# Kernel tuning notes

Measured on AMD Instinct MI355X. Metric: run time of the kernel, lower is better.

Reference implementation:

```python
import jax, jax.numpy as jnp
import numpy as np
from jax import lax

# Production-scale RPN detection-head config
B, FH, FW, NA = 8, 200, 200, 9      # batch, fmap h, fmap w, anchors/cell
H, W = 800, 800                      # image dims
N = FH * FW * NA                     # 360k anchors per image
NMS_THR = 0.7
MIN_SIZE = 1e-3


def _make_anchors():
    scales = np.array([32.0, 64.0, 128.0])
    ratios = np.array([0.5, 1.0, 2.0])
    ws = (scales[:, None] * np.sqrt(1.0 / ratios)[None, :]).reshape(-1)  # [NA]
    hs = (scales[:, None] * np.sqrt(ratios)[None, :]).reshape(-1)
    sy, sx = H / FH, W / FW
    cx = (np.arange(FW) + 0.5) * sx
    cy = (np.arange(FH) + 0.5) * sy
    cxg, cyg = np.meshgrid(cx, cy)                     # [FH,FW]
    cxg = cxg[..., None]; cyg = cyg[..., None]         # [FH,FW,1]
    a = np.stack([cxg - ws / 2, cyg - hs / 2, cxg + ws / 2, cyg + hs / 2], axis=-1)
    return jnp.asarray(a.reshape(-1, 4), jnp.float32)  # [N,4] xyxy


def setup_inputs() -> dict:
    key = jax.random.key(0)
    k1, k2 = jax.random.split(key)
    cls_logits = jax.random.normal(k1, (B, N, 1), jnp.float32)
    reg_deltas = jax.random.normal(k2, (B, N, 4), jnp.float32) * 0.1  # sane exp(dw)
    anchors = jnp.broadcast_to(_make_anchors()[None], (B, N, 4))
    return {
        "cls_logits": cls_logits,
        "reg_deltas": reg_deltas,
        "anchors": anchors,
        "keep_pre_nms": 1000,
        "keep_post_nms": 300,
    }


def _offsets2boxes(deltas, anchors):
    aw = anchors[:, 2] - anchors[:, 0]
    ah = anchors[:, 3] - anchors[:, 1]
    acx = anchors[:, 0] + 0.5 * aw
    acy = anchors[:, 1] + 0.5 * ah
    cx = deltas[:, 0] * aw + acx
    cy = deltas[:, 1] * ah + acy
    w = jnp.exp(deltas[:, 2]) * aw
    h = jnp.exp(deltas[:, 3]) * ah
    return jnp.stack([cx - 0.5 * w, cy - 0.5 * h, cx + 0.5 * w, cy + 0.5 * h], axis=-1)


def _iou_matrix(b):
    area = (b[:, 2] - b[:, 0]) * (b[:, 3] - b[:, 1])
    lt = jnp.maximum(b[:, None, :2], b[None, :, :2])
    rb = jnp.minimum(b[:, None, 2:], b[None, :, 2:])
    wh = jnp.clip(rb - lt, 0.0)
    inter = wh[..., 0] * wh[..., 1]
    return inter / (area[:, None] + area[None, :] - inter + 1e-9)


def _detect_one(logit, delta, anc, pre, post):
    scores = jax.nn.sigmoid(logit.reshape(-1))             # [N]
    boxes = _offsets2boxes(delta.reshape(-1, 4), anc)      # [N,4]
    s, idx = lax.top_k(scores, pre)                        # sorted desc
    b = boxes[idx]                                         # [pre,4]
    # clip to image
    b = jnp.stack([
        jnp.clip(b[:, 0], 0.0, W), jnp.clip(b[:, 1], 0.0, H),
        jnp.clip(b[:, 2], 0.0, W), jnp.clip(b[:, 3], 0.0, H)], axis=-1)
    valid = ((b[:, 2] - b[:, 0]) >= MIN_SIZE) & ((b[:, 3] - b[:, 1]) >= MIN_SIZE)
    # greedy NMS on score-sorted boxes (mask-based, fixed shapes)
    iou = _iou_matrix(lax.stop_gradient(b))                # [pre,pre]
    j = jnp.arange(pre)

    def body(keep, i):
        sup = (iou[i] > NMS_THR) & (j > i) & keep[i]
        return keep & ~sup, None

    keep, _ = lax.scan(body, valid, jnp.arange(pre))
    # compact first `post` kept detections into fixed [post,5], zero-padded
    dets = jnp.concatenate([b, s[:, None]], axis=-1)       # [pre,5]
    rank = jnp.cumsum(keep) - 1
    tgt = jnp.where(keep & (rank < post), rank, post)
    out = jnp.zeros((post + 1, 5), dets.dtype).at[tgt].set(dets)[:post]
    return out


def reference(cls_logits, reg_deltas, anchors, keep_pre_nms, keep_post_nms):
    f = lambda l, d, a: _detect_one(l, d, a, keep_pre_nms, keep_post_nms)
    return jax.vmap(f)(cls_logits, reg_deltas, anchors)    # [B,post,5]
```

## Files before the change

kernel.cpp:

```cpp
#include <hip/hip_runtime.h>
#include <stdint.h>
#include <math.h>

typedef unsigned long long u64;
typedef unsigned int u32;

#define NPI   360000
#define B_IMG 8
#define PRE   1000
#define POST  300
#define CAP   4096
#define NMSF  0.7f
#define IMG_W 800.0f
#define IMG_H 800.0f

#define NBIN    4096
#define KSHIFT  20
#define NGRP    64
#define CHUNK_H 30
#define F4PB_H  (NPI / 4 / CHUNK_H)
#define CHUNK_C 48
#define F4PB_C  (NPI / 4 / CHUNK_C)
#define EPB_C   (NPI / CHUNK_C)
#define LBUF    1024

#define CNT_OFF     0
#define VALID_OFF   256
#define PHIST_OFF   4096
#define PCOARSE_OFF 3936256
#define BOX_OFF     3997696
#define SCORE_OFF   4125696
#define CAND_OFF    4157696
#define MASK_OFF    4419840

#define LDSROWS 496
#define NMS_T   320
#define RBLK    16

__device__ __forceinline__ u32 fkey(float f) {
  u32 u = __float_as_uint(f);
  return (u & 0x80000000u) ? ~u : (u | 0x80000000u);
}
__device__ __forceinline__ u64 rl64(u64 v, int lane) {
  u32 lo = (u32)__builtin_amdgcn_readlane((int)(u32)v, lane);
  u32 hi = (u32)__builtin_amdgcn_readlane((int)(u32)(v >> 32), lane);
  return ((u64)hi << 32) | lo;
}
__device__ __forceinline__ u64 sx64(u64 v, int m) {
  u32 lo = (u32)__shfl_xor((int)(u32)v, m, 64);
  u32 hi = (u32)__shfl_xor((int)(u32)(v >> 32), m, 64);
  return ((u64)hi << 32) | lo;
}

__global__ __launch_bounds__(256) void k_hist(const float* __restrict__ logits,
                                              u32* __restrict__ phist,
                                              u32* __restrict__ pcoarse,
                                              u32* __restrict__ cnt,
                                              u64* __restrict__ validw) {
  __shared__ u32 h[4 * NBIN];
  const int img = blockIdx.y, c = blockIdx.x;
  const int tid = threadIdx.x;
  for (int i = tid; i < 4 * NBIN; i += 256) h[i] = 0;
  __syncthreads();
  const int salt = ((tid >> 4) & 3) * NBIN;
  const float4* L = (const float4*)(logits + (size_t)img * NPI) + (size_t)c * F4PB_H;
  for (int i = tid; i < F4PB_H; i += 256) {
    float4 v = L[i];
    atomicAdd(&h[salt + (fkey(v.x) >> KSHIFT)], 1u);
    atomicAdd(&h[salt + (fkey(v.y) >> KSHIFT)], 1u);
    atomicAdd(&h[salt + (fkey(v.z) >> KSHIFT)], 1u);
    atomicAdd(&h[salt + (fkey(v.w) >> KSHIFT)], 1u);
  }
  __syncthreads();
  u32* P = phist + ((size_t)img * CHUNK_H + c) * NBIN;
  u32* PC = pcoarse + ((size_t)img * CHUNK_H + c) * NGRP;
  const int lane = tid & 63;
#pragma unroll
  for (int k = 0; k < NBIN / 256; k++) {
    int i = k * 256 + tid;
    u32 v = h[i] + h[NBIN + i] + h[2 * NBIN + i] + h[3 * NBIN + i];
    P[i] = v;
    u32 s = v;
#pragma unroll
    for (int m = 1; m < 64; m <<= 1) s += (u32)__shfl_xor((int)s, m, 64);
    if (lane == 0) PC[i >> 6] = s;
  }
  if (c == 0) {
    if (tid < 16) validw[img * 16 + tid] = 0;
    if (img == 0 && tid < B_IMG) cnt[tid] = 0;
  }
}

__global__ __launch_bounds__(256) void k_compact(const float* __restrict__ logits,
                                                 const u32* __restrict__ phist,
                                                 const u32* __restrict__ pcoarse,
                                                 u32* __restrict__ cnt,
                                                 u64* __restrict__ cand) {
  __shared__ u64 buf[LBUF];
  __shared__ u32 bcnt;
  __shared__ u32 gbase;
  __shared__ int stb;
  const int img = blockIdx.y, c = blockIdx.x;
  const int t = threadIdx.x;
  if (t == 0) { bcnt = 0; stb = 0; }
  const float4* L = (const float4*)(logits + (size_t)img * NPI) + (size_t)c * F4PB_C;
  float4 r[8];
#pragma unroll
  for (int k = 0; k < 8; k++) {
    int i = t + k * 256;
    if (i < F4PB_C) r[k] = L[i];
  }
  if (t < 64) {
    const u32* PC = pcoarse + (size_t)img * CHUNK_H * NGRP;
    u32 cg = 0;
    for (int cc = 0; cc < CHUNK_H; cc++) cg += PC[cc * NGRP + t];
    u32 suf = cg;
#pragma unroll
    for (int off = 1; off < 64; off <<= 1) {
      u32 o = (u32)__shfl_down((int)suf, off, 64);
      if (t + off < 64) suf += o;
    }
    u32 sx = suf - cg;
    u64 bal = __ballot(suf >= (u32)PRE && sx < (u32)PRE);
    if (bal) {
      int gc = __builtin_ctzll(bal);
      u32 s_above = (u32)__shfl((int)sx, gc, 64);
      const u32* P = phist + (size_t)img * CHUNK_H * NBIN + gc * (NBIN / NGRP);
      u32 fb = 0;
      for (int cc = 0; cc < CHUNK_H; cc++) fb += P[(size_t)cc * NBIN + t];
      u32 fsuf = fb;
#pragma unroll
      for (int off = 1; off < 64; off <<= 1) {
        u32 o = (u32)__shfl_down((int)fsuf, off, 64);
        if (t + off < 64) fsuf += o;
      }
      u32 fincl = fsuf + s_above;
      u32 fexcl = fincl - fb;
      if (fincl >= (u32)PRE && fexcl < (u32)PRE) stb = gc * (NBIN / NGRP) + t;
    }
  }
  __syncthreads();
  const int tb = stb;
  const int ebase = c * EPB_C;
#pragma unroll
  for (int k = 0; k < 8; k++) {
    int i = t + k * 256;
    if (i < F4PB_C) {
      float xs[4] = {r[k].x, r[k].y, r[k].z, r[k].w};
#pragma unroll
      for (int q = 0; q < 4; q++) {
        float x = xs[q];
        if ((int)(fkey(x) >> KSHIFT) >= tb) {
          float ef = (float)exp(-(double)x);
          float sg = 1.0f / (1.0f + ef);
          u32 e = (u32)(ebase + 4 * i + q);
          u32 p = atomicAdd(&bcnt, 1u);
          if (p < LBUF)
            buf[p] = ((u64)fkey(sg) << 32) | (u64)(0xFFFFFFFFu - e);
        }
      }
    }
  }
  __syncthreads();
  if (t == 0) {
    u32 m = bcnt < LBUF ? bcnt : LBUF;
    bcnt = m;
    gbase = atomicAdd(&cnt[img], m);
  }
  __syncthreads();
  const u32 m = bcnt, gb = gbase;
  for (u32 j = t; j < m; j += 256) {
    u32 pos = gb + j;
    if (pos < CAP) cand[img * CAP + pos] = buf[j];
  }
}

__device__ __forceinline__ void emit_row(
    int img, int row, u64 key,
    const float* __restrict__ deltas, const float* __restrict__ anchors,
    float4* __restrict__ boxes, float* __restrict__ scores, u64* __restrict__ validw) {
  u32 hi  = (u32)(key >> 32);
  u32 idx = 0xFFFFFFFFu - (u32)(key & 0xFFFFFFFFu);
  u32 su  = (hi & 0x80000000u) ? (hi ^ 0x80000000u) : ~hi;
  float sc = __uint_as_float(su);
  size_t off = (size_t)img * NPI + idx;
  float4 d = ((const float4*)deltas)[off];
  float4 a = ((const float4*)anchors)[off];
  float aw = a.z - a.x, ah = a.w - a.y;
  float acx = a.x + 0.5f * aw, acy = a.y + 0.5f * ah;
  float cx = d.x * aw + acx, cy = d.y * ah + acy;
  float w = expf(d.z) * aw, h = expf(d.w) * ah;
  float x1 = cx - 0.5f * w, y1 = cy - 0.5f * h;
  float x2 = cx + 0.5f * w, y2 = cy + 0.5f * h;
  x1 = fminf(fmaxf(x1, 0.f), IMG_W);
  y1 = fminf(fmaxf(y1, 0.f), IMG_H);
  x2 = fminf(fmaxf(x2, 0.f), IMG_W);
  y2 = fminf(fmaxf(y2, 0.f), IMG_H);
  boxes[img * PRE + row]  = make_float4(x1, y1, x2, y2);
  scores[img * PRE + row] = sc;
  if (((x2 - x1) >= 1e-3f) && ((y2 - y1) >= 1e-3f))
    atomicOr(&validw[img * 16 + (row >> 6)], 1ull << (row & 63));
}

__global__ __launch_bounds__(256) void k_rank(
    const float* __restrict__ deltas, const float* __restrict__ anchors,
    const u32* __restrict__ cnt, const u64* __restrict__ cand,
    float4* __restrict__ boxes, float* __restrict__ scores, u64* __restrict__ validw) {
  __shared__ u64 skey[CAP];
  __shared__ u32 pc[4][256];
  const int img = blockIdx.y;
  int n = (int)cnt[img];
  if (n > CAP) n = CAP;
  const int base = blockIdx.x * 256;
  if (base >= n) return;
  for (int i = threadIdx.x; i < n; i += 256) skey[i] = cand[img * CAP + i];
  __syncthreads();
  const int w = threadIdx.x >> 6, l = threadIdx.x & 63;
  const int r0 = base + l, r1 = r0 + 64, r2 = r0 + 128, r3 = r0 + 192;
  u64 k0 = (r0 < n) ? skey[r0] : 0ull;
  u64 k1 = (r1 < n) ? skey[r1] : 0ull;
  u64 k2 = (r2 < n) ? skey[r2] : 0ull;
  u64 k3 = (r3 < n) ? skey[r3] : 0ull;
  int c0 = 0, c1 = 0, c2 = 0, c3 = 0;
  const int js = (w * n) >> 2, je = ((w + 1) * n) >> 2;
  for (int j = js; j < je; j++) {
    u64 kj = skey[j];
    c0 += (kj > k0); c1 += (kj > k1); c2 += (kj > k2); c3 += (kj > k3);
  }
  pc[w][l]       = (u32)c0;
  pc[w][l + 64]  = (u32)c1;
  pc[w][l + 128] = (u32)c2;
  pc[w][l + 192] = (u32)c3;
  __syncthreads();
  const int t = threadIdx.x;
  const int rr = base + t;
  if (rr < n) {
    int c = (int)(pc[0][t] + pc[1][t] + pc[2][t] + pc[3][t]);
    if (c < PRE) emit_row(img, c, skey[rr], deltas, anchors, boxes, scores, validw);
  }
}

__global__ __launch_bounds__(1024) void k_iou(const float4* __restrict__ boxes,
                                              u64* __restrict__ mask) {
  __shared__ float4 sb[1024];
  __shared__ float  sa[1024];
  const int img = blockIdx.y;
  const int tid = threadIdx.x;
  {
    float4 b = (tid < PRE) ? boxes[img * PRE + tid]
                           : make_float4(0.f, 0.f, 0.f, 0.f);
    sb[tid] = b;
    sa[tid] = (b.z - b.x) * (b.w - b.y);
  }
  __syncthreads();
  const int lane = tid & 63;
  const int wv   = tid >> 6;
  const int i    = blockIdx.x * 64 + lane;
  const bool rowok = (i < PRE);
  const float4 bi = sb[blockIdx.x * 64 + lane];
  const float  ai = sa[blockIdx.x * 64 + lane];
  const int cbase = wv << 6;
  u64 bits = 0;
#pragma unroll
  for (int k = 0; k < 64; k++) {
    int c = cbase + k;
    float4 bc = sb[c];
    float ac  = sa[c];
    float ltx = fmaxf(bi.x, bc.x), lty = fmaxf(bi.y, bc.y);
    float rbx = fminf(bi.z, bc.z), rby = fminf(bi.w, bc.w);
    float iw = fmaxf(rbx - ltx, 0.f), ih = fmaxf(rby - lty, 0.f);
    float inter = iw * ih;
    float iou = inter / (ai + ac - inter + 1e-9f);
    bits |= (iou > NMSF) ? (1ull << k) : 0ull;
  }
  int d = i - cbase;
  u64 gtmask = (d < 0) ? ~0ull : ((d >= 63) ? 0ull : (~0ull << (d + 1)));
  int rem = PRE - cbase;
  u64 tmask = (rem >= 64) ? ~0ull : ((rem <= 0) ? 0ull : ((1ull << rem) - 1ull));
  bits &= gtmask & tmask;
  if (rowok) mask[((size_t)img * PRE + i) * 16 + wv] = bits;
}

__global__ __launch_bounds__(NMS_T) void k_nms(
    const u64* __restrict__ mask, const u64* __restrict__ validw,
    const float4* __restrict__ boxes, const float* __restrict__ scores,
    float* __restrict__ out) {
  __shared__ u64 smask[LDSROWS * 16];
  __shared__ int skeeplist[POST];
  __shared__ int skept;
  const int img = blockIdx.x;
  const int tid = threadIdx.x;
  const u64* M = mask + (size_t)img * PRE * 16;
  u64 diag[16];
  if (tid < 64) {
#pragma unroll
    for (int cc = 0; cc < 16; cc++) {
      int row = cc * 64 + tid;
      diag[cc] = (row < PRE) ? M[(size_t)row * 16 + cc] : 0ull;
    }
  }
  for (int e = tid; e < LDSROWS * 16; e += NMS_T) smask[e] = M[e];
  __syncthreads();
  if (tid < 64) {
    const int lane = tid;
    const int w = lane & 15, g = lane >> 4;
    u64 rem = ~0ull;
    if (lane < 16) {
      rem = ~validw[img * 16 + lane];
      if (lane == 15) rem |= 0xFFFFFF0000000000ull;
    }
    int kept = 0;
#pragma unroll
    for (int cc = 0; cc < 16; cc++) {
      u64 alive = ~rl64(rem, cc);
      int kept0 = kept;
      while (alive != 0ull && kept < POST) {
        int r = __builtin_ctzll(alive);
        if (lane == 0) skeeplist[kept] = cc * 64 + r;
        kept++;
        u64 sup = rl64(diag[cc], r);
        alive &= ~sup;
        alive &= ~(1ull << r);
      }
      int nc = kept - kept0;
      if (nc > 0 && kept < POST && cc < 15) {
        u64 part = 0;
        for (int j = g; j < nc; j += 4) {
          int row = skeeplist[kept0 + j];
          part |= (row < LDSROWS) ? smask[row * 16 + w] : M[(size_t)row * 16 + w];
        }
        part |= sx64(part, 16);
        part |= sx64(part, 32);
        rem |= part;
      }
      if (kept >= POST) break;
    }
    if (lane == 0) skept = kept;
  }
  __syncthreads();
  if (tid < POST) {
    float4 bx = make_float4(0.f, 0.f, 0.f, 0.f);
    float  sc = 0.f;
    if (tid < skept) {
      int i = skeeplist[tid];
      bx = boxes[img * PRE + i];
      sc = scores[img * PRE + i];
    }
    float* o = out + ((size_t)img * POST + tid) * 5;
    o[0] = bx.x; o[1] = bx.y; o[2] = bx.z; o[3] = bx.w; o[4] = sc;
  }
}

extern "C" void kernel_launch(void* const* d_in, const int* in_sizes, int n_in,
                              void* d_out, int out_size, void* d_ws, size_t ws_size,
                              hipStream_t stream) {
  const float* logits  = (const float*)d_in[0];
  const float* deltas  = (const float*)d_in[1];
  const float* anchors = (const float*)d_in[2];
  float* out = (float*)d_out;
  char* ws = (char*)d_ws;

  u32* cnt      = (u32*)(ws + CNT_OFF);
  u64* validw   = (u64*)(ws + VALID_OFF);
  u32* phist    = (u32*)(ws + PHIST_OFF);
  u32* pcoarse  = (u32*)(ws + PCOARSE_OFF);
  float4* boxes = (float4*)(ws + BOX_OFF);
  float* scores = (float*)(ws + SCORE_OFF);
  u64* cand     = (u64*)(ws + CAND_OFF);
  u64* mask     = (u64*)(ws + MASK_OFF);

  dim3 gh(CHUNK_H, B_IMG);
  k_hist<<<gh, 256, 0, stream>>>(logits, phist, pcoarse, cnt, validw);
  dim3 gc(CHUNK_C, B_IMG);
  k_compact<<<gc, 256, 0, stream>>>(logits, phist, pcoarse, cnt, cand);
  dim3 gr(RBLK, B_IMG);
  k_rank<<<gr, 256, 0, stream>>>(deltas, anchors, cnt, cand, boxes, scores, validw);
  dim3 g2(16, B_IMG);
  k_iou<<<g2, 1024, 0, stream>>>(boxes, mask);
  k_nms<<<B_IMG, NMS_T, 0, stream>>>(mask, validw, boxes, scores, out);
}
```

Before: 210.2 us.

## Replace histogram threshold pass with fixed logit threshold and exact fallback

Removes the per-image histogram kernel. Candidates are now selected with a fixed logit threshold and written into per-block buffers. The rank kernel gathers these buffers, and if any block overflows or the total falls outside the range needed for the top 1000, it rebuilds the exact histogram and threshold in-kernel. The IoU kernel is re-gridded to 32-row blocks and zeroes mask words strictly below the diagonal without computing them. This cuts a full pass over the logits and a launch, at the cost of a slow single-block fallback if the input distribution differs.

New measurement: 200.4 us. -4.7%, faster.

```diff
diff --git a/kernel.cpp b/kernel.cpp
--- a/kernel.cpp
+++ b/kernel.cpp
@@ -17,21 +17,19 @@
 #define NBIN    4096
 #define KSHIFT  20
 #define NGRP    64
-#define CHUNK_H 30
-#define F4PB_H  (NPI / 4 / CHUNK_H)
 #define CHUNK_C 48
 #define F4PB_C  (NPI / 4 / CHUNK_C)
 #define EPB_C   (NPI / CHUNK_C)
-#define LBUF    1024
-
-#define CNT_OFF     0
+#define PBLK    128
+
+#define THR_LOGIT 2.62f
+
 #define VALID_OFF   256
-#define PHIST_OFF   4096
-#define PCOARSE_OFF 3936256
-#define BOX_OFF     3997696
-#define SCORE_OFF   4125696
-#define CAND_OFF    4157696
-#define MASK_OFF    4419840
+#define BCNT_OFF    4096
+#define PCAND_OFF   8192
+#define BOX_OFF     401408
+#define SCORE_OFF   529408
+#define MASK_OFF    561408
 
 #define LDSROWS 496
 #define NMS_T   320
@@ -52,127 +50,42 @@
   return ((u64)hi << 32) | lo;
 }
 
-__global__ __launch_bounds__(256) void k_hist(const float* __restrict__ logits,
-                                              u32* __restrict__ phist,
-                                              u32* __restrict__ pcoarse,
-                                              u32* __restrict__ cnt,
-                                              u64* __restrict__ validw) {
-  __shared__ u32 h[4 * NBIN];
-  const int img = blockIdx.y, c = blockIdx.x;
-  const int tid = threadIdx.x;
-  for (int i = tid; i < 4 * NBIN; i += 256) h[i] = 0;
-  __syncthreads();
-  const int salt = ((tid >> 4) & 3) * NBIN;
-  const float4* L = (const float4*)(logits + (size_t)img * NPI) + (size_t)c * F4PB_H;
-  for (int i = tid; i < F4PB_H; i += 256) {
-    float4 v = L[i];
-    atomicAdd(&h[salt + (fkey(v.x) >> KSHIFT)], 1u);
-    atomicAdd(&h[salt + (fkey(v.y) >> KSHIFT)], 1u);
-    atomicAdd(&h[salt + (fkey(v.z) >> KSHIFT)], 1u);
-    atomicAdd(&h[salt + (fkey(v.w) >> KSHIFT)], 1u);
-  }
-  __syncthreads();
-  u32* P = phist + ((size_t)img * CHUNK_H + c) * NBIN;
-  u32* PC = pcoarse + ((size_t)img * CHUNK_H + c) * NGRP;
-  const int lane = tid & 63;
-#pragma unroll
-  for (int k = 0; k < NBIN / 256; k++) {
-    int i = k * 256 + tid;
-    u32 v = h[i] + h[NBIN + i] + h[2 * NBIN + i] + h[3 * NBIN + i];
-    P[i] = v;
-    u32 s = v;
-#pragma unroll
-    for (int m = 1; m < 64; m <<= 1) s += (u32)__shfl_xor((int)s, m, 64);
-    if (lane == 0) PC[i >> 6] = s;
-  }
-  if (c == 0) {
-    if (tid < 16) validw[img * 16 + tid] = 0;
-    if (img == 0 && tid < B_IMG) cnt[tid] = 0;
-  }
-}
-
 __global__ __launch_bounds__(256) void k_compact(const float* __restrict__ logits,
-                                                 const u32* __restrict__ phist,
-                                                 const u32* __restrict__ pcoarse,
-                                                 u32* __restrict__ cnt,
-                                                 u64* __restrict__ cand) {
-  __shared__ u64 buf[LBUF];
+                                                 u32* __restrict__ bcnt_blk,
+                                                 u64* __restrict__ pcand,
+                                                 u64* __restrict__ validw) {
   __shared__ u32 bcnt;
-  __shared__ u32 gbase;
-  __shared__ int stb;
   const int img = blockIdx.y, c = blockIdx.x;
   const int t = threadIdx.x;
-  if (t == 0) { bcnt = 0; stb = 0; }
+  const u32 FK0 = fkey(THR_LOGIT);
+  if (t == 0) bcnt = 0;
+  if (c == 0 && t < 16) validw[img * 16 + t] = 0;
+  __syncthreads();
   const float4* L = (const float4*)(logits + (size_t)img * NPI) + (size_t)c * F4PB_C;
-  float4 r[8];
-#pragma unroll
-  for (int k = 0; k < 8; k++) {
-    int i = t + k * 256;
-    if (i < F4PB_C) r[k] = L[i];
-  }
-  if (t < 64) {
-    const u32* PC = pcoarse + (size_t)img * CHUNK_H * NGRP;
-    u32 cg = 0;
-    for (int cc = 0; cc < CHUNK_H; cc++) cg += PC[cc * NGRP + t];
-    u32 suf = cg;
-#pragma unroll
-    for (int off = 1; off < 64; off <<= 1) {
-      u32 o = (u32)__shfl_down((int)suf, off, 64);
-      if (t + off < 64) suf += o;
-    }
-    u32 sx = suf - cg;
-    u64 bal = __ballot(suf >= (u32)PRE && sx < (u32)PRE);
-    if (bal) {
-      int gc = __builtin_ctzll(bal);
-      u32 s_above = (u32)__shfl((int)sx, gc, 64);
-      const u32* P = phist + (size_t)img * CHUNK_H * NBIN + gc * (NBIN / NGRP);
-      u32 fb = 0;
-      for (int cc = 0; cc < CHUNK_H; cc++) fb += P[(size_t)cc * NBIN + t];
-      u32 fsuf = fb;
-#pragma unroll
-      for (int off = 1; off < 64; off <<= 1) {
-        u32 o = (u32)__shfl_down((int)fsuf, off, 64);
-        if (t + off < 64) fsuf += o;
-      }
-      u32 fincl = fsuf + s_above;
-      u32 fexcl = fincl - fb;
-      if (fincl >= (u32)PRE && fexcl < (u32)PRE) stb = gc * (NBIN / NGRP) + t;
-    }
-  }
-  __syncthreads();
-  const int tb = stb;
+  u64* P = pcand + ((size_t)img * CHUNK_C + c) * PBLK;
   const int ebase = c * EPB_C;
 #pragma unroll
   for (int k = 0; k < 8; k++) {
     int i = t + k * 256;
     if (i < F4PB_C) {
-      float xs[4] = {r[k].x, r[k].y, r[k].z, r[k].w};
+      float4 v = L[i];
+      float xs[4] = {v.x, v.y, v.z, v.w};
 #pragma unroll
       for (int q = 0; q < 4; q++) {
         float x = xs[q];
-        if ((int)(fkey(x) >> KSHIFT) >= tb) {
+        if (fkey(x) >= FK0) {
           float ef = (float)exp(-(double)x);
           float sg = 1.0f / (1.0f + ef);
           u32 e = (u32)(ebase + 4 * i + q);
           u32 p = atomicAdd(&bcnt, 1u);
-          if (p < LBUF)
-            buf[p] = ((u64)fkey(sg) << 32) | (u64)(0xFFFFFFFFu - e);
+          if (p < PBLK)
+            P[p] = ((u64)fkey(sg) << 32) | (u64)(0xFFFFFFFFu - e);
         }
       }
     }
   }
   __syncthreads();
-  if (t == 0) {
-    u32 m = bcnt < LBUF ? bcnt : LBUF;
-    bcnt = m;
-    gbase = atomicAdd(&cnt[img], m);
-  }
-  __syncthreads();
-  const u32 m = bcnt, gb = gbase;
-  for (u32 j = t; j < m; j += 256) {
-    u32 pos = gb + j;
-    if (pos < CAP) cand[img * CAP + pos] = buf[j];
-  }
+  if (t == 0) bcnt_blk[img * CHUNK_C + c] = bcnt;
 }
 
 __device__ __forceinline__ void emit_row(
@@ -203,19 +116,114 @@
 }
 
 __global__ __launch_bounds__(256) void k_rank(
+    const float* __restrict__ logits,
     const float* __restrict__ deltas, const float* __restrict__ anchors,
-    const u32* __restrict__ cnt, const u64* __restrict__ cand,
+    const u32* __restrict__ bcnt_blk, const u64* __restrict__ pcand,
     float4* __restrict__ boxes, float* __restrict__ scores, u64* __restrict__ validw) {
   __shared__ u64 skey[CAP];
   __shared__ u32 pc[4][256];
+  __shared__ u32 scnt[CHUNK_C], soff[CHUNK_C];
+  __shared__ int sn, sbad, stb;
+  __shared__ u32 rc;
   const int img = blockIdx.y;
-  int n = (int)cnt[img];
-  if (n > CAP) n = CAP;
+  const int tid = threadIdx.x;
+  const int w = tid >> 6, l = tid & 63;
+  if (tid < CHUNK_C) scnt[tid] = bcnt_blk[img * CHUNK_C + tid];
+  if (tid == 0) { sbad = 0; stb = 0; rc = 0; }
+  __syncthreads();
+  if (tid < 64) {
+    u32 m = (tid < CHUNK_C) ? (scnt[tid] > (u32)PBLK ? (u32)PBLK : scnt[tid]) : 0u;
+    u64 bb = __ballot(tid < CHUNK_C && scnt[tid] > (u32)PBLK);
+    u32 x = m;
+#pragma unroll
+    for (int off = 1; off < 64; off <<= 1) {
+      u32 o = (u32)__shfl_up((int)x, off, 64);
+      if (l >= off) x += o;
+    }
+    if (tid < CHUNK_C) soff[tid] = x - m;
+    u32 tot = (u32)__builtin_amdgcn_readlane((int)x, 63);
+    if (tid == 0) {
+      sn = (int)tot;
+      if (bb != 0ull || tot < (u32)PRE || tot > (u32)CAP) sbad = 1;
+    }
+  }
+  __syncthreads();
+  int n = sn;
+  if (!sbad) {
+    for (int c = w; c < CHUNK_C; c += 4) {
+      u32 mc = scnt[c];
+      u32 off = soff[c];
+      const u64* src = pcand + ((size_t)img * CHUNK_C + c) * PBLK;
+      for (u32 j = l; j < mc; j += 64) skey[off + j] = src[j];
+    }
+    __syncthreads();
+  } else {
+    u32* hh = (u32*)skey;
+    for (int i = tid; i < NBIN; i += 256) hh[i] = 0;
+    __syncthreads();
+    const float4* L = (const float4*)(logits + (size_t)img * NPI);
+    for (int i = tid; i < NPI / 4; i += 256) {
+      float4 v = L[i];
+      atomicAdd(&hh[fkey(v.x) >> KSHIFT], 1u);
+      atomicAdd(&hh[fkey(v.y) >> KSHIFT], 1u);
+      atomicAdd(&hh[fkey(v.z) >> KSHIFT], 1u);
+      atomicAdd(&hh[fkey(v.w) >> KSHIFT], 1u);
+    }
+    __syncthreads();
+    if (tid < 64) {
+      u32 cg = 0;
+      for (int b = 0; b < NBIN / NGRP; b++) cg += hh[tid * (NBIN / NGRP) + b];
+      u32 suf = cg;
+#pragma unroll
+      for (int off = 1; off < 64; off <<= 1) {
+        u32 o = (u32)__shfl_down((int)suf, off, 64);
+        if (tid + off < 64) suf += o;
+      }
+      u32 sx = suf - cg;
+      u64 bal = __ballot(suf >= (u32)PRE && sx < (u32)PRE);
+      if (bal) {
+        int gc = __builtin_ctzll(bal);
+        u32 s_above = (u32)__shfl((int)sx, gc, 64);
+        u32 fb = hh[gc * (NBIN / NGRP) + tid];
+        u32 fsuf = fb;
+#pragma unroll
+        for (int off = 1; off < 64; off <<= 1) {
+          u32 o = (u32)__shfl_down((int)fsuf, off, 64);
+          if (tid + off < 64) fsuf += o;
+        }
+        u32 fincl = fsuf + s_above, fexcl = fincl - fb;
+        if (fincl >= (u32)PRE && fexcl < (u32)PRE) stb = gc * (NBIN / NGRP) + tid;
+      }
+    }
+    __syncthreads();
+    const int tb = stb;
+    for (int i = tid; i < NPI / 4; i += 256) {
+      float4 v = L[i];
+      float xs[4] = {v.x, v.y, v.z, v.w};
+#pragma unroll
+      for (int q = 0; q < 4; q++) {
+        float x = xs[q];
+        if ((int)(fkey(x) >> KSHIFT) >= tb) {
+          float ef = (float)exp(-(double)x);
+          float sg = 1.0f / (1.0f + ef);
+          u32 e = (u32)(4 * i + q);
+          u32 p = atomicAdd(&rc, 1u);
+          if (p < CAP) skey[p] = ((u64)fkey(sg) << 32) | (u64)(0xFFFFFFFFu - e);
+        }
+      }
+    }
+    __syncthreads();
+    n = (int)(rc < (u32)CAP ? rc : (u32)CAP);
+    for (int r = tid; r < n; r += 256) {
+      u64 kr = skey[r];
+      int cr = 0;
+      for (int j = 0; j < n; j++) cr += (skey[j] > kr);
+      if (cr < PRE) emit_row(img, cr, kr, deltas, anchors, boxes, scores, validw);
+    }
+    return;
+  }
   const int base = blockIdx.x * 256;
   if (base >= n) return;
-  for (int i = threadIdx.x; i < n; i += 256) skey[i] = cand[img * CAP + i];
-  __syncthreads();
-  const int w = threadIdx.x >> 6, l = threadIdx.x & 63;
   const int r0 = base + l, r1 = r0 + 64, r2 = r0 + 128, r3 = r0 + 192;
   u64 k0 = (r0 < n) ? skey[r0] : 0ull;
   u64 k1 = (r1 < n) ? skey[r1] : 0ull;
@@ -232,34 +240,35 @@
   pc[w][l + 128] = (u32)c2;
   pc[w][l + 192] = (u32)c3;
   __syncthreads();
-  const int t = threadIdx.x;
-  const int rr = base + t;
+  const int rr = base + tid;
   if (rr < n) {
-    int c = (int)(pc[0][t] + pc[1][t] + pc[2][t] + pc[3][t]);
+    int c = (int)(pc[0][tid] + pc[1][tid] + pc[2][tid] + pc[3][tid]);
     if (c < PRE) emit_row(img, c, skey[rr], deltas, anchors, boxes, scores, validw);
   }
 }
 
-__global__ __launch_bounds__(1024) void k_iou(const float4* __restrict__ boxes,
-                                              u64* __restrict__ mask) {
+__global__ __launch_bounds__(512) void k_iou(const float4* __restrict__ boxes,
+                                             u64* __restrict__ mask) {
   __shared__ float4 sb[1024];
   __shared__ float  sa[1024];
-  const int img = blockIdx.y;
+  const int img = blockIdx.y, rb = blockIdx.x;
   const int tid = threadIdx.x;
-  {
-    float4 b = (tid < PRE) ? boxes[img * PRE + tid]
-                           : make_float4(0.f, 0.f, 0.f, 0.f);
-    sb[tid] = b;
-    sa[tid] = (b.z - b.x) * (b.w - b.y);
-  }
-  __syncthreads();
-  const int lane = tid & 63;
-  const int wv   = tid >> 6;
-  const int i    = blockIdx.x * 64 + lane;
+  for (int j = tid; j < 1024; j += 512) {
+    float4 b = (j < PRE) ? boxes[img * PRE + j] : make_float4(0.f, 0.f, 0.f, 0.f);
+    sb[j] = b;
+    sa[j] = (b.z - b.x) * (b.w - b.y);
+  }
+  __syncthreads();
+  const int i  = rb * 32 + (tid & 31);
+  const int wv = tid >> 5;
   const bool rowok = (i < PRE);
-  const float4 bi = sb[blockIdx.x * 64 + lane];
-  const float  ai = sa[blockIdx.x * 64 + lane];
   const int cbase = wv << 6;
+  if (cbase + 63 < rb * 32) {
+    if (rowok) mask[((size_t)img * PRE + i) * 16 + wv] = 0ull;
+    return;
+  }
+  const float4 bi = sb[i];
+  const float  ai = sa[i];
   u64 bits = 0;
 #pragma unroll
   for (int k = 0; k < 64; k++) {
@@ -360,22 +369,19 @@
   float* out = (float*)d_out;
   char* ws = (char*)d_ws;
 
-  u32* cnt      = (u32*)(ws + CNT_OFF);
   u64* validw   = (u64*)(ws + VALID_OFF);
-  u32* phist    = (u32*)(ws + PHIST_OFF);
-  u32* pcoarse  = (u32*)(ws + PCOARSE_OFF);
+  u32* bcnt_blk = (u32*)(ws + BCNT_OFF);
+  u64* pcand    = (u64*)(ws + PCAND_OFF);
   float4* boxes = (float4*)(ws + BOX_OFF);
   float* scores = (float*)(ws + SCORE_OFF);
-  u64* cand     = (u64*)(ws + CAND_OFF);
   u64* mask     = (u64*)(ws + MASK_OFF);
 
-  dim3 gh(CHUNK_H, B_IMG);
-  k_hist<<<gh, 256, 0, stream>>>(logits, phist, pcoarse, cnt, validw);
   dim3 gc(CHUNK_C, B_IMG);
-  k_compact<<<gc, 256, 0, stream>>>(logits, phist, pcoarse, cnt, cand);
+  k_compact<<<gc, 256, 0, stream>>>(logits, bcnt_blk, pcand, validw);
   dim3 gr(RBLK, B_IMG);
-  k_rank<<<gr, 256, 0, stream>>>(deltas, anchors, cnt, cand, boxes, scores, validw);
-  dim3 g2(16, B_IMG);
-  k_iou<<<g2, 1024, 0, stream>>>(boxes, mask);
+  k_rank<<<gr, 256, 0, stream>>>(logits, deltas, anchors, bcnt_blk, pcand,
+                                 boxes, scores, validw);
+  dim3 g2(32, B_IMG);
+  k_iou<<<g2, 512, 0, stream>>>(boxes, mask);
   k_nms<<<B_IMG, NMS_T, 0, stream>>>(mask, validw, boxes, scores, out);
 }
```
